# Kernel optimization log

Hardware: AMD Instinct MI355X
Metric: run time of the kernel (lower is better)

## Reference

```python
import math
import jax, jax.numpy as jnp
import numpy as np

B, T, D, H = 2, 2048, 2048, 16
Dh = D // H


def setup_inputs() -> dict:
    key = jax.random.key(0)
    k1, k2, k3, k4, k5 = jax.random.split(key, 5)
    scale = 1.0 / math.sqrt(D)
    return {
        "x": jax.random.normal(k1, (B, T, D), dtype=jnp.float32),
        "Wqkv": jax.random.normal(k2, (D, 3 * D), dtype=jnp.float32) * scale,
        "bqkv": jax.random.normal(k3, (3 * D,), dtype=jnp.float32) * 0.01,
        "Wout": jax.random.normal(k4, (D, D), dtype=jnp.float32) * scale,
        "bout": jax.random.normal(k5, (D,), dtype=jnp.float32) * 0.01,
    }


def reference(x, Wqkv, bqkv, Wout, bout):
    b, t, d = x.shape
    # QKV projection: [B,T,3D] -> [B,T,3,H,Dh]
    qkv = (x @ Wqkv + bqkv).reshape(b, t, 3, H, Dh)
    q, k, v = qkv[:, :, 0], qkv[:, :, 1], qkv[:, :, 2]  # each [B,T,H,Dh]
    # scores: [B,H,Tq,Tk]
    attn = jnp.einsum("bqhd,bkhd->bhqk", q, k) / math.sqrt(Dh)
    causal = jnp.tril(jnp.ones((t, t), dtype=bool))  # T_total == T_new (no cache)
    attn = jnp.where(causal[None, None], attn, -jnp.inf)
    attn = jax.nn.softmax(attn, axis=-1)
    out = jnp.einsum("bhqk,bkhd->bqhd", attn, v).reshape(b, t, d)
    return out @ Wout + bout
```

## Files before the change

### kernel.cpp

```cpp
#include <hip/hip_runtime.h>

typedef _Float16 f16;
typedef _Float16 f16x8 __attribute__((ext_vector_type(8)));
typedef _Float16 f16x4 __attribute__((ext_vector_type(4)));
typedef float f32x4 __attribute__((ext_vector_type(4)));

#define B_ 2
#define T_ 2048
#define D_ 2048
#define H_ 16
#define DH_ 128

__global__ void f32_to_f16_k(const float* __restrict__ in, f16* __restrict__ out, int n4) {
    int i = blockIdx.x * blockDim.x + threadIdx.x;
    if (i < n4) {
        float4 v = *((const float4*)in + i);
        f16x4 h;
        h[0] = (f16)v.x; h[1] = (f16)v.y; h[2] = (f16)v.z; h[3] = (f16)v.w;
        *((f16x4*)out + i) = h;
    }
}

__global__ void transpose_f32_to_f16_k(const float* __restrict__ in, f16* __restrict__ out,
                                       int R, int C) {
    __shared__ float tile[32][33];
    int c0 = blockIdx.x * 32, r0 = blockIdx.y * 32;
    int tx = threadIdx.x, ty = threadIdx.y;
#pragma unroll
    for (int j = 0; j < 4; j++)
        tile[ty + j * 8][tx] = in[(size_t)(r0 + ty + j * 8) * C + c0 + tx];
    __syncthreads();
#pragma unroll
    for (int j = 0; j < 4; j++)
        out[(size_t)(c0 + ty + j * 8) * R + r0 + tx] = (f16)tile[tx][ty + j * 8];
}

__device__ __forceinline__ void gload_lds16(const f16* g, f16* l) {
    __builtin_amdgcn_global_load_lds(
        (const __attribute__((address_space(1))) void*)g,
        (__attribute__((address_space(3))) void*)l, 16, 0, 0);
}

template <int MODE>
__global__ __launch_bounds__(256) void gemm_k(
    const f16* __restrict__ A, const f16* __restrict__ Bt,
    const float* __restrict__ bias,
    f16* __restrict__ Qo, f16* __restrict__ Ko, f16* __restrict__ Vto,
    float* __restrict__ Co) {
    const int m0 = blockIdx.y * 128, n0 = blockIdx.x * 128;
    const int tid = threadIdx.x;
    const int w = tid >> 6, lane = tid & 63;
    const int wr = w >> 1, wc = w & 1;
    const int lr = lane & 15, hi = lane >> 4, lk8 = (lane >> 4) * 8;
    const int srow = lane >> 2, scol = (lane & 3) * 8;

    __shared__ f16 As[128][32];
    __shared__ f16 Bs[128][32];

    f32x4 acc[4][4] = {};

    const f16* Ab = A + (size_t)m0 * 2048;
    const f16* Bb = Bt + (size_t)n0 * 2048;

    for (int k0 = 0; k0 < 2048; k0 += 32) {
        __syncthreads();
#pragma unroll
        for (int c = 0; c < 2; c++) {
            int ch = w * 2 + c;
            gload_lds16(Ab + (size_t)(ch * 16 + srow) * 2048 + k0 + scol, &As[ch * 16][0]);
            gload_lds16(Bb + (size_t)(ch * 16 + srow) * 2048 + k0 + scol, &Bs[ch * 16][0]);
        }
        __syncthreads();
        f16x8 a[4], b[4];
#pragma unroll
        for (int m = 0; m < 4; m++) a[m] = *(const f16x8*)&As[wr * 64 + m * 16 + lr][lk8];
#pragma unroll
        for (int n = 0; n < 4; n++) b[n] = *(const f16x8*)&Bs[wc * 64 + n * 16 + lr][lk8];
#pragma unroll
        for (int m = 0; m < 4; m++)
#pragma unroll
            for (int n = 0; n < 4; n++)
                acc[m][n] = __builtin_amdgcn_mfma_f32_16x16x32_f16(a[m], b[n], acc[m][n], 0, 0, 0);
    }

    const float qscale = 0.08838834764831845f * 1.44269504088896340736f;
#pragma unroll
    for (int m = 0; m < 4; m++) {
        int row_l = wr * 64 + m * 16 + hi * 4;
#pragma unroll
        for (int n = 0; n < 4; n++) {
            int col = n0 + wc * 64 + n * 16 + lr;
            float bv = bias[col];
#pragma unroll
            for (int i = 0; i < 4; i++) {
                int row = m0 + row_l + i;
                float v = acc[m][n][i] + bv;
                if (MODE == 0) {
                    int sqkv = col >> 11;
                    int r = col & 2047;
                    int h = r >> 7, dh = r & 127;
                    int bb = row >> 11, t = row & 2047;
                    if (sqkv == 0) {
                        Qo[((size_t)(bb * H_ + h) * T_ + t) * DH_ + dh] = (f16)(v * qscale);
                    } else if (sqkv == 1) {
                        Ko[((size_t)(bb * H_ + h) * T_ + t) * DH_ + dh] = (f16)v;
                    } else {
                        Vto[((size_t)(bb * H_ + h) * DH_ + dh) * T_ + t] = (f16)v;
                    }
                } else {
                    Co[(size_t)row * 2048 + col] = v;
                }
            }
        }
    }
}

__global__ __launch_bounds__(256, 3) void attn_k(
    const f16* __restrict__ Q, const f16* __restrict__ K,
    const f16* __restrict__ Vt, f16* __restrict__ O) {
    const int tid = threadIdx.x;
    const int w = tid >> 6, lane = tid & 63;
    const int lr = lane & 15, hi = lane >> 4, lk8 = hi * 8;

    const int bid = blockIdx.x;
    const int half = bid >> 8, idx = bid & 255;
    const int bh = half * 16 + (idx >> 4);
    const int g = half ? (15 - (idx & 15)) : (idx & 15);
    const int qb = g * 128;
    const int nt = (g + 1) * 4;

    const f16* Qp = Q + (size_t)bh * T_ * DH_;
    const f16* Kp = K + (size_t)bh * T_ * DH_;
    const f16* Vp = Vt + (size_t)bh * DH_ * T_;

    __shared__ f16 Ks[2][4096];
    __shared__ f16 Vs[2][4096];
    __shared__ f16 Pl[4][32][40];

    const int krow0 = w * 8 + (lane >> 4);
    const int kcol = ((lane & 15) * 16);
    const int vrow0 = w * 32 + (lane >> 2);
    const int vcol = ((lane & 3) * 16);

    f16x8 qf[2][4];
#pragma unroll
    for (int r = 0; r < 2; r++)
#pragma unroll
        for (int kc = 0; kc < 4; kc++)
            qf[r][kc] = *(const f16x8*)&Qp[(size_t)(qb + w * 32 + r * 16 + lr) * DH_ + kc * 32 + lk8];

    f32x4 accO[2][8] = {};
    float lsum[2] = {0.f, 0.f};

    {
#pragma unroll
        for (int is = 0; is < 2; is++) {
            int row = krow0 + is * 4;
            gload_lds16(Kp + (size_t)row * DH_ + ((kcol ^ ((row & 7) << 4)) >> 1),
                        &Ks[0][w * 1024 + is * 512]);
        }
#pragma unroll
        for (int is = 0; is < 2; is++) {
            int row = vrow0 + is * 16;
            gload_lds16(Vp + (size_t)row * T_ + ((vcol ^ ((row & 3) << 4)) >> 1),
                        &Vs[0][w * 1024 + is * 512]);
        }
    }
    __syncthreads();

    int cur = 0;
    for (int t = 0; t < nt; ++t) {
        const int kt = t * 32;
        if (t + 1 < nt) {
            const int ktn = kt + 32;
#pragma unroll
            for (int is = 0; is < 2; is++) {
                int row = krow0 + is * 4;
                gload_lds16(Kp + (size_t)(ktn + row) * DH_ + ((kcol ^ ((row & 7) << 4)) >> 1),
                            &Ks[cur ^ 1][w * 1024 + is * 512]);
            }
#pragma unroll
            for (int is = 0; is < 2; is++) {
                int row = vrow0 + is * 16;
                gload_lds16(Vp + (size_t)row * T_ + ktn + ((vcol ^ ((row & 3) << 4)) >> 1),
                            &Vs[cur ^ 1][w * 1024 + is * 512]);
            }
        }
        const f16* KsC = &Ks[cur][0];
        const f16* VsC = &Vs[cur][0];

        f32x4 s[2][2] = {};
#pragma unroll
        for (int kc = 0; kc < 4; kc++) {
            const int swz = ((kc * 64 + hi * 16) ^ ((lr & 7) << 4)) >> 1;
            f16x8 kf0 = *(const f16x8*)&KsC[(0 * 16 + lr) * 128 + swz];
            f16x8 kf1 = *(const f16x8*)&KsC[(1 * 16 + lr) * 128 + swz];
#pragma unroll
            for (int r = 0; r < 2; r++) {
                s[r][0] = __builtin_amdgcn_mfma_f32_16x16x32_f16(kf0, qf[r][kc], s[r][0], 0, 0, 0);
                s[r][1] = __builtin_amdgcn_mfma_f32_16x16x32_f16(kf1, qf[r][kc], s[r][1], 0, 0, 0);
            }
        }
        if (t >= nt - 4) {
#pragma unroll
            for (int r = 0; r < 2; r++) {
                const int q = qb + w * 32 + r * 16 + lr;
#pragma unroll
                for (int i = 0; i < 4; i++) {
                    if (kt + hi * 4 + i > q)      s[r][0][i] = -1e30f;
                    if (kt + 16 + hi * 4 + i > q) s[r][1][i] = -1e30f;
                }
            }
        }
#pragma unroll
        for (int r = 0; r < 2; r++) {
            f16x4 a, b;
#pragma unroll
            for (int i = 0; i < 4; i++) {
                float p0 = __builtin_exp2f(s[r][0][i]);
                float p1 = __builtin_exp2f(s[r][1][i]);
                lsum[r] += p0 + p1;
                a[i] = (f16)p0; b[i] = (f16)p1;
            }
            *(f16x4*)&Pl[w][r * 16 + lr][hi * 4] = a;
            *(f16x4*)&Pl[w][r * 16 + lr][16 + hi * 4] = b;
        }
        f16x8 pa0 = *(const f16x8*)&Pl[w][lr][lk8];
        f16x8 pa1 = *(const f16x8*)&Pl[w][16 + lr][lk8];
#pragma unroll
        for (int n = 0; n < 8; n++) {
            const int vr = n * 16 + lr;
            f16x8 vf = *(const f16x8*)&VsC[vr * 32 + ((hi * 16 ^ ((lr & 3) << 4)) >> 1)];
            accO[0][n] = __builtin_amdgcn_mfma_f32_16x16x32_f16(vf, pa0, accO[0][n], 0, 0, 0);
            accO[1][n] = __builtin_amdgcn_mfma_f32_16x16x32_f16(vf, pa1, accO[1][n], 0, 0, 0);
        }
        __syncthreads();
        cur ^= 1;
    }

    const int bb = bh >> 4, hh = bh & 15;
#pragma unroll
    for (int r = 0; r < 2; r++) {
        float l = lsum[r];
        l += __shfl_xor(l, 16);
        l += __shfl_xor(l, 32);
        const float linv = 1.0f / l;
        size_t rowbase = ((size_t)(bb * T_ + qb + w * 32 + r * 16 + lr)) * D_ + hh * DH_;
#pragma unroll
        for (int n = 0; n < 8; n++) {
            f16x4 h4;
#pragma unroll
            for (int i = 0; i < 4; i++) h4[i] = (f16)(accO[r][n][i] * linv);
            *(f16x4*)&O[rowbase + n * 16 + hi * 4] = h4;
        }
    }
}

extern "C" void kernel_launch(void* const* d_in, const int* in_sizes, int n_in,
                              void* d_out, int out_size, void* d_ws, size_t ws_size,
                              hipStream_t stream) {
    const float* x    = (const float*)d_in[0];
    const float* Wqkv = (const float*)d_in[1];
    const float* bqkv = (const float*)d_in[2];
    const float* Wout = (const float*)d_in[3];
    const float* bout = (const float*)d_in[4];
    float* out = (float*)d_out;

    char* ws = (char*)d_ws;
    f16* xh    = (f16*)(ws);
    f16* wqkvt = (f16*)(ws + 16777216);
    f16* woutt = (f16*)(ws + 41943040);
    f16* Qb    = (f16*)(ws + 50331648);
    f16* Kb    = (f16*)(ws + 67108864);
    f16* Vtb   = (f16*)(ws + 83886080);
    f16* Oh    = xh;

    f32_to_f16_k<<<8192, 256, 0, stream>>>(x, xh, (B_ * T_ * D_) / 4);
    transpose_f32_to_f16_k<<<dim3(192, 64), dim3(32, 8), 0, stream>>>(Wqkv, wqkvt, 2048, 6144);
    transpose_f32_to_f16_k<<<dim3(64, 64), dim3(32, 8), 0, stream>>>(Wout, woutt, 2048, 2048);

    gemm_k<0><<<dim3(48, 32), 256, 0, stream>>>(xh, wqkvt, bqkv, Qb, Kb, Vtb, nullptr);

    attn_k<<<512, 256, 0, stream>>>(Qb, Kb, Vtb, Oh);

    gemm_k<1><<<dim3(16, 32), 256, 0, stream>>>(Oh, woutt, bout, nullptr, nullptr, nullptr, out);
}
```

Baseline: 425.9 us.

## Replace QKV GEMM with 256x256 8-wave double-buffered ping-pong kernel

The QKV projection GEMM moves from 128x128 tiles with 4 waves and single-buffered LDS to 256x256 tiles with 8 waves. The new kernel uses XOR-swizzled, double-buffered LDS stages with a K-step of 64, and interleaves global-to-LDS loads with MFMA phases using barriers, setprio and explicit vmcnt waits. The aim is to hide global load latency and raise MFMA utilisation for the largest GEMM. In exchange it uses 128KB of LDS per block, launches only 384 blocks, and depends on fragile manual scheduling. The output GEMM is split into its own simplified kernel.

```diff
diff --git a/kernel.cpp b/kernel.cpp
--- a/kernel.cpp
+++ b/kernel.cpp
@@ -41,12 +41,156 @@
         (__attribute__((address_space(3))) void*)l, 16, 0, 0);
 }
 
-template <int MODE>
-__global__ __launch_bounds__(256) void gemm_k(
+#define PH_PRE                                              \
+    asm volatile("" ::: "memory");                          \
+    __builtin_amdgcn_s_barrier();                           \
+    asm volatile("s_waitcnt lgkmcnt(0)" ::: "memory");      \
+    __builtin_amdgcn_sched_barrier(0);                      \
+    __builtin_amdgcn_s_setprio(1)
+#define PH_POST                                             \
+    __builtin_amdgcn_s_setprio(0);                          \
+    asm volatile("" ::: "memory");                          \
+    __builtin_amdgcn_s_barrier();                           \
+    asm volatile("" ::: "memory")
+
+__global__ __launch_bounds__(512, 2) void gemm_qkv8_k(
     const f16* __restrict__ A, const f16* __restrict__ Bt,
     const float* __restrict__ bias,
-    f16* __restrict__ Qo, f16* __restrict__ Ko, f16* __restrict__ Vto,
-    float* __restrict__ Co) {
+    f16* __restrict__ Qo, f16* __restrict__ Ko, f16* __restrict__ Vto) {
+    const int m0 = blockIdx.y * 256, n0 = blockIdx.x * 256;
+    const int tid = threadIdx.x;
+    const int w = tid >> 6, lane = tid & 63;
+    const int wm = w >> 2, wn = w & 3;
+    const int lr = lane & 15, hi = lane >> 4;
+    const int l8 = lane >> 3, l7 = lane & 7;
+
+    __shared__ f16 sm[65536];
+
+    const f16* Ab = A + (size_t)m0 * 2048;
+    const f16* Bb = Bt + (size_t)n0 * 2048;
+
+    f32x4 acc[8][4] = {};
+    f16x8 afA[4][2], afB[4][2], bf[4][2];
+
+    const int scol = (l7 ^ l8) << 3;
+    const int sw = (lr & 7) << 4;
+
+#define STG(gp, ldsbase, kt, h)                                               \
+    do {                                                                      \
+        _Pragma("unroll")                                                     \
+        for (int c = 0; c < 2; c++) {                                         \
+            const int rl = (h) * 128 + w * 16 + c * 8;                        \
+            gload_lds16((gp) + (size_t)(rl + l8) * 2048 + (kt) * 64 + scol,   \
+                        &sm[(ldsbase) + rl * 64]);                            \
+        }                                                                     \
+    } while (0)
+
+    auto lda = [&](f16x8(&dst)[4][2], int aoff, int mbase) {
+#pragma unroll
+        for (int mm = 0; mm < 4; mm++) {
+            const int base = aoff + (wm * 128 + (mbase + mm) * 16 + lr) * 64;
+#pragma unroll
+            for (int kk = 0; kk < 2; kk++)
+                dst[mm][kk] = *(const f16x8*)&sm[base + (((kk * 64 + hi * 16) ^ sw) >> 1)];
+        }
+    };
+    auto ldb = [&](int boff, int nbase) {
+#pragma unroll
+        for (int nn = 0; nn < 2; nn++) {
+            const int base = boff + (wn * 64 + (nbase + nn) * 16 + lr) * 64;
+#pragma unroll
+            for (int kk = 0; kk < 2; kk++)
+                bf[nbase + nn][kk] = *(const f16x8*)&sm[base + (((kk * 64 + hi * 16) ^ sw) >> 1)];
+        }
+    };
+    auto mfma8 = [&](f16x8(&af)[4][2], int mbase, int nbase) {
+#pragma unroll
+        for (int mm = 0; mm < 4; mm++)
+#pragma unroll
+            for (int nn = 0; nn < 2; nn++)
+#pragma unroll
+                for (int kk = 0; kk < 2; kk++)
+                    acc[mbase + mm][nbase + nn] = __builtin_amdgcn_mfma_f32_16x16x32_f16(
+                        af[mm][kk], bf[nbase + nn][kk], acc[mbase + mm][nbase + nn], 0, 0, 0);
+    };
+
+    STG(Ab, 0, 0, 0);     STG(Ab, 0, 0, 1);
+    STG(Bb, 32768, 0, 0); STG(Bb, 32768, 0, 1);
+    STG(Bb, 49152, 1, 0); STG(Bb, 49152, 1, 1);
+    asm volatile("s_waitcnt vmcnt(4)" ::: "memory");
+    __builtin_amdgcn_s_barrier();
+    asm volatile("" ::: "memory");
+
+#pragma unroll 1
+    for (int i = 0; i < 16; ++i) {
+        const int k2 = 2 * i;
+        const bool nl = (i < 15);
+        lda(afA, 0, 0); ldb(32768, 0);
+        STG(Ab, 16384, k2 + 1, 0);
+        PH_PRE; mfma8(afA, 0, 0); PH_POST;
+        ldb(32768, 2);
+        STG(Ab, 16384, k2 + 1, 1);
+        PH_PRE; mfma8(afA, 0, 2); PH_POST;
+        lda(afB, 0, 4);
+        if (nl) STG(Bb, 32768, k2 + 2, 0);
+        PH_PRE; mfma8(afB, 4, 0); PH_POST;
+        if (nl) STG(Bb, 32768, k2 + 2, 1);
+        PH_PRE; mfma8(afB, 4, 2);
+        __builtin_amdgcn_s_setprio(0);
+        if (nl) asm volatile("s_waitcnt vmcnt(4)" ::: "memory");
+        else    asm volatile("s_waitcnt vmcnt(0)" ::: "memory");
+        asm volatile("" ::: "memory");
+        __builtin_amdgcn_s_barrier();
+        asm volatile("" ::: "memory");
+        lda(afA, 16384, 0); ldb(49152, 0);
+        if (nl) STG(Ab, 0, k2 + 2, 0);
+        PH_PRE; mfma8(afA, 0, 0); PH_POST;
+        ldb(49152, 2);
+        if (nl) STG(Ab, 0, k2 + 2, 1);
+        PH_PRE; mfma8(afA, 0, 2); PH_POST;
+        lda(afB, 16384, 4);
+        if (nl) STG(Bb, 49152, k2 + 3, 0);
+        PH_PRE; mfma8(afB, 4, 0); PH_POST;
+        if (nl) STG(Bb, 49152, k2 + 3, 1);
+        PH_PRE; mfma8(afB, 4, 2);
+        __builtin_amdgcn_s_setprio(0);
+        if (nl) asm volatile("s_waitcnt vmcnt(4)" ::: "memory");
+        asm volatile("" ::: "memory");
+        __builtin_amdgcn_s_barrier();
+        asm volatile("" ::: "memory");
+    }
+#undef STG
+
+    const float qscale = 0.08838834764831845f * 1.44269504088896340736f;
+#pragma unroll
+    for (int n = 0; n < 4; n++) {
+        const int col = n0 + wn * 64 + n * 16 + lr;
+        const float bv = bias[col];
+        const int sqkv = col >> 11;
+        const int rr = col & 2047;
+        const int hh = rr >> 7, dh = rr & 127;
+#pragma unroll
+        for (int m = 0; m < 8; m++) {
+            const int row_l = wm * 128 + m * 16 + hi * 4;
+#pragma unroll
+            for (int i2 = 0; i2 < 4; i2++) {
+                const int row = m0 + row_l + i2;
+                const int bb = row >> 11, t = row & 2047;
+                const float v = acc[m][n][i2] + bv;
+                if (sqkv == 0)
+                    Qo[((size_t)(bb * H_ + hh) * T_ + t) * DH_ + dh] = (f16)(v * qscale);
+                else if (sqkv == 1)
+                    Ko[((size_t)(bb * H_ + hh) * T_ + t) * DH_ + dh] = (f16)v;
+                else
+                    Vto[((size_t)(bb * H_ + hh) * DH_ + dh) * T_ + t] = (f16)v;
+            }
+        }
+    }
+}
+
+__global__ __launch_bounds__(256) void gemm_out_k(
+    const f16* __restrict__ A, const f16* __restrict__ Bt,
+    const float* __restrict__ bias, float* __restrict__ Co) {
     const int m0 = blockIdx.y * 128, n0 = blockIdx.x * 128;
     const int tid = threadIdx.x;
     const int w = tid >> 6, lane = tid & 63;
@@ -83,7 +227,6 @@
                 acc[m][n] = __builtin_amdgcn_mfma_f32_16x16x32_f16(a[m], b[n], acc[m][n], 0, 0, 0);
     }
 
-    const float qscale = 0.08838834764831845f * 1.44269504088896340736f;
 #pragma unroll
     for (int m = 0; m < 4; m++) {
         int row_l = wr * 64 + m * 16 + hi * 4;
@@ -92,25 +235,8 @@
             int col = n0 + wc * 64 + n * 16 + lr;
             float bv = bias[col];
 #pragma unroll
-            for (int i = 0; i < 4; i++) {
-                int row = m0 + row_l + i;
-                float v = acc[m][n][i] + bv;
-                if (MODE == 0) {
-                    int sqkv = col >> 11;
-                    int r = col & 2047;
-                    int h = r >> 7, dh = r & 127;
-                    int bb = row >> 11, t = row & 2047;
-                    if (sqkv == 0) {
-                        Qo[((size_t)(bb * H_ + h) * T_ + t) * DH_ + dh] = (f16)(v * qscale);
-                    } else if (sqkv == 1) {
-                        Ko[((size_t)(bb * H_ + h) * T_ + t) * DH_ + dh] = (f16)v;
-                    } else {
-                        Vto[((size_t)(bb * H_ + h) * DH_ + dh) * T_ + t] = (f16)v;
-                    }
-                } else {
-                    Co[(size_t)row * 2048 + col] = v;
-                }
-            }
+            for (int i = 0; i < 4; i++)
+                Co[(size_t)(m0 + row_l + i) * 2048 + col] = acc[m][n][i] + bv;
         }
     }
 }
@@ -279,9 +405,9 @@
     transpose_f32_to_f16_k<<<dim3(192, 64), dim3(32, 8), 0, stream>>>(Wqkv, wqkvt, 2048, 6144);
     transpose_f32_to_f16_k<<<dim3(64, 64), dim3(32, 8), 0, stream>>>(Wout, woutt, 2048, 2048);
 
-    gemm_k<0><<<dim3(48, 32), 256, 0, stream>>>(xh, wqkvt, bqkv, Qb, Kb, Vtb, nullptr);
+    gemm_qkv8_k<<<dim3(24, 16), 512, 0, stream>>>(xh, wqkvt, bqkv, Qb, Kb, Vtb);
 
     attn_k<<<512, 256, 0, stream>>>(Qb, Kb, Vtb, Oh);
 
-    gemm_k<1><<<dim3(16, 32), 256, 0, stream>>>(Oh, woutt, bout, nullptr, nullptr, nullptr, out);
-}
+    gemm_out_k<<<dim3(16, 32), 256, 0, stream>>>(Oh, woutt, bout, out);
+}
```

Result: faster. 408.3 us (-4.1%).
